# Kernel tuning notes

Measured on AMD Instinct MI355X. Metric: run time of the kernel, lower is better.

Reference implementation:

```python
import jax, jax.numpy as jnp
import numpy as np

N = 4096      # nodes (= attention seq_len)
D = 256       # dim_h
H = 4         # num_heads
HD = D // H   # head dim
E = 131072    # edges (avg degree 32)


def _ln(x, g, b, eps=1e-5):
    mu = jnp.mean(x, -1, keepdims=True)
    var = jnp.var(x, -1, keepdims=True)
    return (x - mu) * jax.lax.rsqrt(var + eps) * g + b


def setup_inputs() -> dict:
    key = jax.random.key(0)
    ks = jax.random.split(key, 10)
    s = 0.02
    nrm = lambda k, shape: jax.random.normal(k, shape, jnp.float32) * s
    return dict(
        x=jax.random.normal(ks[0], (N, D), jnp.float32),
        edge_index=jax.random.randint(ks[1], (2, E), 0, N, dtype=jnp.int32),
        W_gcn=nrm(ks[2], (D, D)), b_gcn=jnp.zeros((D,), jnp.float32),
        w_qkv=nrm(ks[3], (D, 3 * D)), b_qkv=jnp.zeros((3 * D,), jnp.float32),
        w_out=nrm(ks[4], (D, D)), b_out=jnp.zeros((D,), jnp.float32),
        g1l=jnp.ones((D,), jnp.float32), beta1l=jnp.zeros((D,), jnp.float32),
        g1a=jnp.ones((D,), jnp.float32), beta1a=jnp.zeros((D,), jnp.float32),
        W1=nrm(ks[5], (D, 2 * D)), bf1=jnp.zeros((2 * D,), jnp.float32),
        W2=nrm(ks[6], (2 * D, D)), bf2=jnp.zeros((D,), jnp.float32),
        g2=jnp.ones((D,), jnp.float32), beta2=jnp.zeros((D,), jnp.float32),
    )


def reference(x, edge_index, W_gcn, b_gcn, w_qkv, b_qkv, w_out, b_out,
              g1l, beta1l, g1a, beta1a, W1, bf1, W2, bf2, g2, beta2):
    n = x.shape[0]
    # --- GCNConv: sym-normalized aggregation with self loops ---
    loop = jnp.arange(n, dtype=edge_index.dtype)
    src = jnp.concatenate([edge_index[0], loop])
    dst = jnp.concatenate([edge_index[1], loop])
    deg = jax.ops.segment_sum(jnp.ones_like(src, x.dtype), dst, num_segments=n)
    dinv = jax.lax.rsqrt(deg)  # deg >= 1 thanks to self loops
    h = x @ W_gcn                                  # [N, D]
    msg = h[src] * (dinv[src] * dinv[dst])[:, None]  # gather + edge norm
    x_local = jax.ops.segment_sum(msg, dst, num_segments=n) + b_gcn
    x = _ln(x + x_local, g1l, beta1l)
    # --- Multi-head self-attention over all nodes (one sequence) ---
    qkv = x @ w_qkv + b_qkv
    q, k, v = jnp.split(qkv, 3, axis=-1)
    q = q.reshape(n, H, HD)
    k = k.reshape(n, H, HD)
    v = v.reshape(n, H, HD)
    scale = 1.0 / (HD ** 0.5)
    scores = jnp.einsum('nhd,mhd->hnm', q, k) * scale   # [H, N, N]
    attn = jax.nn.softmax(scores, axis=-1)
    x_attn = jnp.einsum('hnm,mhd->nhd', attn, v).reshape(n, D) @ w_out + b_out
    x = _ln(x + x_attn, g1a, beta1a)
    # --- FFN (D -> 2D -> D, ReLU) ---
    x_ffn = jax.nn.relu(x @ W1 + bf1) @ W2 + bf2
    return _ln(x + x_ffn, g2, beta2)
```

## Files before the change

kernel.cpp:

```cpp
#include <hip/hip_runtime.h>

typedef unsigned short u16;
typedef __bf16 bf16x8 __attribute__((ext_vector_type(8)));
typedef float f32x4 __attribute__((ext_vector_type(4)));

__device__ __forceinline__ u16 f2u(float f) {
    unsigned u = __builtin_bit_cast(unsigned, f);
    return (u16)((u + 0x7FFFu + ((u >> 16) & 1u)) >> 16);
}

__device__ __forceinline__ float u2f(u16 h) {
    return __builtin_bit_cast(float, (unsigned)h << 16);
}

__device__ __forceinline__ void glds16(const u16* g, u16* l) {
    __builtin_amdgcn_global_load_lds((const __attribute__((address_space(1))) unsigned int*)g,
                                     (__attribute__((address_space(3))) unsigned int*)l, 16, 0, 0);
}


__global__ __launch_bounds__(256) void prep_k(
    const float* __restrict__ w0, const float* __restrict__ w1, const float* __restrict__ w2,
    const float* __restrict__ w3, const float* __restrict__ w4, const float* __restrict__ x,
    u16* __restrict__ o0, u16* __restrict__ o1, u16* __restrict__ o2,
    u16* __restrict__ o3, u16* __restrict__ o4, u16* __restrict__ xo,
    int* __restrict__ cnt, int xblocks, int nn) {
    int b = blockIdx.x, t = threadIdx.x;
    if (b < 144) {
        const float* in; u16* out; int R, C, tb;
        if (b < 16)       { in = w0; out = o0; R = 256; C = 256; tb = b; }
        else if (b < 64)  { in = w1; out = o1; R = 256; C = 768; tb = b - 16; }
        else if (b < 80)  { in = w2; out = o2; R = 256; C = 256; tb = b - 64; }
        else if (b < 112) { in = w3; out = o3; R = 256; C = 512; tb = b - 80; }
        else              { in = w4; out = o4; R = 512; C = 256; tb = b - 112; }
        int tcols = C >> 6;
        int tr = tb / tcols, tc = tb - tr * tcols;
        __shared__ float T[64][65];
        int i0 = t >> 6, j = t & 63;
#pragma unroll
        for (int p = 0; p < 16; p++) {
            int r = p * 4 + i0;
            T[r][j] = in[(long)(tr * 64 + r) * C + tc * 64 + j];
        }
        __syncthreads();
#pragma unroll
        for (int p = 0; p < 16; p++) {
            int c = p * 4 + i0;
            out[(long)(tc * 64 + c) * R + tr * 64 + j] = f2u(T[j][c]);
        }
    } else if (b < 144 + xblocks) {
        long base = (long)(b - 144) * 4096;
#pragma unroll
        for (int p = 0; p < 4; p++) {
            long idx = base + p * 1024 + t * 4;
            float4 v = *(const float4*)&x[idx];
            unsigned lo = (unsigned)f2u(v.x) | ((unsigned)f2u(v.y) << 16);
            unsigned hi = (unsigned)f2u(v.z) | ((unsigned)f2u(v.w) << 16);
            *(uint2*)&xo[idx] = uint2{lo, hi};
        }
    } else {
        int i = (b - 144 - xblocks) * 256 + t;
        if (i < nn) cnt[i] = 0;
    }
}


__device__ __forceinline__ void block_ln_stats(float v, float& mu, float& rstd) {
    float s1 = v, s2 = v * v;
#pragma unroll
    for (int m = 1; m < 64; m <<= 1) { s1 += __shfl_xor(s1, m, 64); s2 += __shfl_xor(s2, m, 64); }
    __shared__ float r1[4], r2[4];
    int lane = threadIdx.x & 63, w = threadIdx.x >> 6;
    if (lane == 0) { r1[w] = s1; r2[w] = s2; }
    __syncthreads();
    s1 = r1[0] + r1[1] + r1[2] + r1[3];
    s2 = r2[0] + r2[1] + r2[2] + r2[3];
    mu = s1 * (1.0f / 256.0f);
    float var = s2 * (1.0f / 256.0f) - mu * mu;
    rstd = rsqrtf(var + 1e-5f);
}


__global__ __launch_bounds__(256) void gcn_agg_ln_k(
    const u16* __restrict__ h, const float* __restrict__ x,
    const int* __restrict__ srcs, const int* __restrict__ cnt,
    const float* __restrict__ bg,
    const float* __restrict__ g, const float* __restrict__ be,
    float* __restrict__ x1, u16* __restrict__ x1bf) {
    int n = blockIdx.x, d = threadIdx.x;
    int c = cnt[n]; c = c < 128 ? c : 128;
    int st = n << 7;
    float dn = rsqrtf((float)(c + 1));
    float agg = u2f(h[(long)n * 256 + d]) * dn;
    int e = 0;
    for (; e + 4 <= c; e += 4) {
        int s0 = srcs[st + e], s1 = srcs[st + e + 1], s2 = srcs[st + e + 2], s3 = srcs[st + e + 3];
        float a0 = u2f(h[(long)s0 * 256 + d]) * rsqrtf((float)(cnt[s0] + 1));
        float a1 = u2f(h[(long)s1 * 256 + d]) * rsqrtf((float)(cnt[s1] + 1));
        float a2 = u2f(h[(long)s2 * 256 + d]) * rsqrtf((float)(cnt[s2] + 1));
        float a3 = u2f(h[(long)s3 * 256 + d]) * rsqrtf((float)(cnt[s3] + 1));
        agg += (a0 + a1) + (a2 + a3);
    }
    for (; e < c; e++) {
        int s = srcs[st + e];
        agg += u2f(h[(long)s * 256 + d]) * rsqrtf((float)(cnt[s] + 1));
    }
    float v = x[(long)n * 256 + d] + dn * agg + bg[d];
    float mu, rs;
    block_ln_stats(v, mu, rs);
    float y = (v - mu) * rs * g[d] + be[d];
    x1[(long)n * 256 + d] = y;
    x1bf[(long)n * 256 + d] = f2u(y);
}


template <int EPI>
__device__ __forceinline__ void gemm_body(
    int bx, int by,
    const u16* __restrict__ A, const u16* __restrict__ Bt,
    const float* __restrict__ bias, void* __restrict__ outp,
    int M, int N, int K) {
    __shared__ __align__(16) u16 As[64 * 256];
    __shared__ __align__(16) u16 Bs[64 * 256];
    int tid = threadIdx.x;
    int lane = tid & 63, w = tid >> 6;
    int l15 = lane & 15, quad = lane >> 4, l7 = l15 & 7;
    int m0 = bx * 64, n0 = by * 64;
    int wm = (w >> 1) * 32, wn = (w & 1) * 32;
    f32x4 acc[2][2];
#pragma unroll
    for (int i = 0; i < 2; i++)
#pragma unroll
        for (int j = 0; j < 2; j++) acc[i][j] = f32x4{0.f, 0.f, 0.f, 0.f};

    int rA0 = (wm + l15) * 256, rA1 = (wm + 16 + l15) * 256;
    int rB0 = (wn + l15) * 256, rB1 = (wn + 16 + l15) * 256;

    for (int kb = 0; kb < K; kb += 256) {
        if (kb) __syncthreads();
#pragma unroll
        for (int i = 0; i < 8; i++) {
            int s = i * 256 + tid;
            int j = s >> 5, dch = s & 31;
            int c = dch ^ (j & 7);
            glds16(A + (long)(m0 + j) * K + kb + c * 8, &As[s * 8]);
            glds16(Bt + (long)(n0 + j) * K + kb + c * 8, &Bs[s * 8]);
        }
        __syncthreads();
#pragma unroll
        for (int step = 0; step < 8; step++) {
            int d8 = (((step << 2) + quad) ^ l7) << 3;
            bf16x8 af0 = *(const bf16x8*)&As[rA0 + d8];
            bf16x8 af1 = *(const bf16x8*)&As[rA1 + d8];
            bf16x8 bf0 = *(const bf16x8*)&Bs[rB0 + d8];
            bf16x8 bf1 = *(const bf16x8*)&Bs[rB1 + d8];
            acc[0][0] = __builtin_amdgcn_mfma_f32_16x16x32_bf16(af0, bf0, acc[0][0], 0, 0, 0);
            acc[0][1] = __builtin_amdgcn_mfma_f32_16x16x32_bf16(af0, bf1, acc[0][1], 0, 0, 0);
            acc[1][0] = __builtin_amdgcn_mfma_f32_16x16x32_bf16(af1, bf0, acc[1][0], 0, 0, 0);
            acc[1][1] = __builtin_amdgcn_mfma_f32_16x16x32_bf16(af1, bf1, acc[1][1], 0, 0, 0);
        }
    }

#pragma unroll
    for (int nf = 0; nf < 2; nf++) {
        int col = n0 + wn + nf * 16 + l15;
        float bv = bias ? bias[col] : 0.0f;
#pragma unroll
        for (int mf = 0; mf < 2; mf++) {
#pragma unroll
            for (int r = 0; r < 4; r++) {
                int row = m0 + wm + mf * 16 + quad * 4 + r;
                float v = acc[mf][nf][r] + bv;
                if (EPI == 1) {
                    u16* q = (u16*)outp;
                    u16* kk = q + (long)M * 256;
                    u16* vt = kk + (long)M * 256;
                    if (col < 256) {
                        q[(((col >> 6) * (long)M) + row) * 64 + (col & 63)] = f2u(v * 0.180336884f);
                    } else if (col < 512) {
                        int c = col - 256;
                        kk[(((c >> 6) * (long)M) + row) * 64 + (c & 63)] = f2u(v);
                    } else {
                        int c = col - 512;
                        vt[((c >> 6) * 64 + (c & 63)) * (long)M + row] = f2u(v);
                    }
                } else if (EPI == 2) {
                    ((u16*)outp)[(long)row * N + col] = f2u(v > 0.f ? v : 0.f);
                } else {
                    ((u16*)outp)[(long)row * N + col] = f2u(v);
                }
            }
        }
    }
}

template <int EPI>
__global__ __launch_bounds__(256) void gemm_k(
    const u16* __restrict__ A, const u16* __restrict__ Bt,
    const float* __restrict__ bias, void* __restrict__ outp,
    int M, int N, int K) {
    gemm_body<EPI>(blockIdx.x, blockIdx.y, A, Bt, bias, outp, M, N, K);
}


template <int WRITE_BF>
__global__ __launch_bounds__(256) void gemm_ln_k(
    const u16* __restrict__ A, const u16* __restrict__ Bt, const float* __restrict__ bias,
    const float* __restrict__ res, const float* __restrict__ g, const float* __restrict__ be,
    float* __restrict__ outf, u16* __restrict__ outbf, int M, int K) {
    __shared__ __align__(16) u16 As[16 * 64];
    __shared__ __align__(16) u16 Bs[256 * 64];
    __shared__ float red[2][4][16];
    int tid = threadIdx.x;
    int lane = tid & 63, w = tid >> 6;
    int l15 = lane & 15, quad = lane >> 4, l7 = l15 & 7;
    int m0 = blockIdx.x * 16;
    f32x4 acc[4];
#pragma unroll
    for (int i = 0; i < 4; i++) acc[i] = f32x4{0.f, 0.f, 0.f, 0.f};

    int jA = tid >> 3, dA = tid & 7, cA = dA ^ (jA & 7);
    const u16* agp = A + (long)(m0 + jA) * K + cA * 8;

    for (int kb = 0; kb < K; kb += 64) {
        if (kb) __syncthreads();
        if (tid < 128) glds16(agp + kb, &As[tid * 8]);
#pragma unroll
        for (int i = 0; i < 8; i++) {
            int s = i * 256 + tid;
            int jb = s >> 3, db = s & 7, cb = db ^ (jb & 7);
            glds16(Bt + (long)jb * K + kb + cb * 8, &Bs[s * 8]);
        }
        __syncthreads();
#pragma unroll
        for (int step = 0; step < 2; step++) {
            int d8 = (((step << 2) + quad) ^ l7) << 3;
            bf16x8 af = *(const bf16x8*)&As[l15 * 64 + d8];
#pragma unroll
            for (int nf = 0; nf < 4; nf++) {
                int rb = w * 64 + nf * 16 + l15;
                bf16x8 bfr = *(const bf16x8*)&Bs[rb * 64 + d8];
                acc[nf] = __builtin_amdgcn_mfma_f32_16x16x32_bf16(af, bfr, acc[nf], 0, 0, 0);
            }
        }
    }

    float vv[4][4];
    float p1[4] = {0.f, 0.f, 0.f, 0.f}, p2[4] = {0.f, 0.f, 0.f, 0.f};
#pragma unroll
    for (int nf = 0; nf < 4; nf++) {
        int col = w * 64 + nf * 16 + l15;
        float bv = bias[col];
#pragma unroll
        for (int r = 0; r < 4; r++) {
            int row = m0 + quad * 4 + r;
            float v = acc[nf][r] + bv + res[(long)row * 256 + col];
            vv[nf][r] = v;
            p1[r] += v; p2[r] += v * v;
        }
    }
#pragma unroll
    for (int m = 1; m < 16; m <<= 1) {
#pragma unroll
        for (int r = 0; r < 4; r++) {
            p1[r] += __shfl_xor(p1[r], m, 64);
            p2[r] += __shfl_xor(p2[r], m, 64);
        }
    }
    if (l15 == 0) {
#pragma unroll
        for (int r = 0; r < 4; r++) { red[0][w][quad * 4 + r] = p1[r]; red[1][w][quad * 4 + r] = p2[r]; }
    }
    __syncthreads();
    float mu[4], rs[4];
#pragma unroll
    for (int r = 0; r < 4; r++) {
        int rr = quad * 4 + r;
        float s1 = red[0][0][rr] + red[0][1][rr] + red[0][2][rr] + red[0][3][rr];
        float s2 = red[1][0][rr] + red[1][1][rr] + red[1][2][rr] + red[1][3][rr];
        mu[r] = s1 * (1.0f / 256.0f);
        float var = s2 * (1.0f / 256.0f) - mu[r] * mu[r];
        rs[r] = rsqrtf(var + 1e-5f);
    }
#pragma unroll
    for (int nf = 0; nf < 4; nf++) {
        int col = w * 64 + nf * 16 + l15;
        float gg = g[col], bb = be[col];
#pragma unroll
        for (int r = 0; r < 4; r++) {
            int row = m0 + quad * 4 + r;
            float y = (vv[nf][r] - mu[r]) * rs[r] * gg + bb;
            outf[(long)row * 256 + col] = y;
            if (WRITE_BF) outbf[(long)row * 256 + col] = f2u(y);
        }
    }
}


__global__ __launch_bounds__(256) void front_k(
    const int* __restrict__ ei, int E, int* __restrict__ cnt, int* __restrict__ srcs,
    const u16* __restrict__ A, const u16* __restrict__ Bt, void* __restrict__ outp,
    int M, int N, int K, int SB) {
    int b = blockIdx.x;
    if (b < SB) {
        int e = b * 256 + threadIdx.x;
        if (e < E) {
            int s = ei[e], d = ei[E + e];
            int p = atomicAdd(&cnt[d], 1);
            if (p < 128) srcs[(d << 7) + p] = s;
        }
    } else {
        int id = b - SB;
        gemm_body<3>(id & 63, id >> 6, A, Bt, nullptr, outp, M, N, K);
    }
}


__global__ __launch_bounds__(256) void attn_k(const u16* __restrict__ qg, const u16* __restrict__ kg,
                                              const u16* __restrict__ vtg, float* __restrict__ po,
                                              float* __restrict__ pl, int N, int S) {
    int tid = threadIdx.x;
    int w = tid >> 6, lane = tid & 63, l15 = lane & 15, quad = lane >> 4;
    int lid = blockIdx.x + 64 * blockIdx.y + 256 * blockIdx.z;
    int hs = lid & 7;
    int hh = hs & 3, sp = hs >> 2, qb = lid >> 3;
    int q0 = qb * 64 + w * 16;
    int kbeg = sp * (N / S);
    int nit = (N / S) / 64;
    const u16* qh = qg + (long)hh * N * 64;
    const u16* kh = kg + (long)hh * N * 64;
    const u16* vh = vtg + (long)hh * 64 * N;

    __shared__ __align__(16) u16 KV[2][2][4096];
    __shared__ __align__(16) u16 P[4][1024];
    u16* Pw = &P[w][0];

    int s0 = tid, j0 = s0 >> 3, c0s = ((s0 & 7) ^ (j0 & 7)) * 8;
    int s1 = tid + 256, j1 = s1 >> 3, c1s = ((s1 & 7) ^ (j1 & 7)) * 8;
    const u16* kp0 = kh + (long)(kbeg + j0) * 64 + c0s;
    const u16* kp1 = kh + (long)(kbeg + j1) * 64 + c1s;
    const u16* vp0 = vh + (long)j0 * N + kbeg + c0s;
    const u16* vp1 = vh + (long)j1 * N + kbeg + c1s;
    u16* lk0[2] = {&KV[0][0][s0 * 8], &KV[1][0][s0 * 8]};
    u16* lk1[2] = {&KV[0][0][s1 * 8], &KV[1][0][s1 * 8]};
    u16* lv0[2] = {&KV[0][1][s0 * 8], &KV[1][1][s0 * 8]};
    u16* lv1[2] = {&KV[0][1][s1 * 8], &KV[1][1][s1 * 8]};

    int lo3 = l15 & 7;
    int c0 = (quad ^ lo3) * 8;
    int c1 = c0 ^ 32;
    int ps = lo3 << 1;
    int pw0 = l15 * 64 + (((quad << 1) ^ ps) << 2);
    int pw1 = l15 * 64 + (((8 + (quad << 1)) ^ ps) << 2);
    int pca[4];
#pragma unroll
    for (int nt = 0; nt < 4; nt++) pca[nt] = l15 * 64 + (((nt * 4 + quad) ^ ps) << 2);

    bf16x8 aq0 = *(const bf16x8*)(qh + (long)(q0 + l15) * 64 + quad * 8);
    bf16x8 aq1 = *(const bf16x8*)(qh + (long)(q0 + l15) * 64 + 32 + quad * 8);
    bf16x8 ones;
#pragma unroll
    for (int i = 0; i < 8; i++) ones[i] = (__bf16)1.0f;

    f32x4 o[4];
#pragma unroll
    for (int dn = 0; dn < 4; dn++) o[dn] = f32x4{0.f, 0.f, 0.f, 0.f};
    f32x4 accl = f32x4{0.f, 0.f, 0.f, 0.f};

    glds16(kp0, lk0[0]); glds16(kp1, lk1[0]);
    glds16(vp0, lv0[0]); glds16(vp1, lv1[0]);
    kp0 += 4096; kp1 += 4096; vp0 += 64; vp1 += 64;

    for (int it = 0; it < nit; it++) {
        __syncthreads();
        if (it + 1 < nit) {
            int nb = (it + 1) & 1;
            glds16(kp0, lk0[nb]); glds16(kp1, lk1[nb]);
            glds16(vp0, lv0[nb]); glds16(vp1, lv1[nb]);
            kp0 += 4096; kp1 += 4096; vp0 += 64; vp1 += 64;
        }
        const u16* Kc = &KV[it & 1][0][0];
        const u16* Vc = &KV[it & 1][1][0];
#pragma unroll
        for (int nt = 0; nt < 4; nt++) {
            const u16* Kr = Kc + (nt * 16 + l15) * 64;
            bf16x8 kf0 = *(const bf16x8*)(Kr + c0);
            bf16x8 kf1 = *(const bf16x8*)(Kr + c1);
            f32x4 s = f32x4{0.f, 0.f, 0.f, 0.f};
            s = __builtin_amdgcn_mfma_f32_16x16x32_bf16(kf0, aq0, s, 0, 0, 0);
            s = __builtin_amdgcn_mfma_f32_16x16x32_bf16(kf1, aq1, s, 0, 0, 0);
            unsigned u0 = (unsigned)((int)(s[0] * 8388608.0f) + 1064992209);
            unsigned u1 = (unsigned)((int)(s[1] * 8388608.0f) + 1064992209);
            unsigned u2 = (unsigned)((int)(s[2] * 8388608.0f) + 1064992209);
            unsigned u3 = (unsigned)((int)(s[3] * 8388608.0f) + 1064992209);
            unsigned pk01 = __builtin_amdgcn_perm(u1, u0, 0x07060302u);
            unsigned pk23 = __builtin_amdgcn_perm(u3, u2, 0x07060302u);
            *(uint2*)&Pw[pca[nt]] = uint2{pk01, pk23};
        }
        bf16x8 pa0 = *(const bf16x8*)&Pw[pw0];
        bf16x8 pa1 = *(const bf16x8*)&Pw[pw1];
        accl = __builtin_amdgcn_mfma_f32_16x16x32_bf16(pa0, ones, accl, 0, 0, 0);
        accl = __builtin_amdgcn_mfma_f32_16x16x32_bf16(pa1, ones, accl, 0, 0, 0);
#pragma unroll
        for (int dn = 0; dn < 4; dn++) {
            const u16* Vr = Vc + (dn * 16 + l15) * 64;
            bf16x8 v0 = *(const bf16x8*)(Vr + c0);
            bf16x8 v1 = *(const bf16x8*)(Vr + c1);
            o[dn] = __builtin_amdgcn_mfma_f32_16x16x32_bf16(pa0, v0, o[dn], 0, 0, 0);
            o[dn] = __builtin_amdgcn_mfma_f32_16x16x32_bf16(pa1, v1, o[dn], 0, 0, 0);
        }
    }

    long pbase = ((long)(sp * 4 + hh)) * N;
#pragma unroll
    for (int dn = 0; dn < 4; dn++)
#pragma unroll
        for (int r = 0; r < 4; r++) {
            int row = q0 + quad * 4 + r;
            po[(pbase + row) * 64 + dn * 16 + l15] = o[dn][r];
        }
    if (l15 == 0) {
#pragma unroll
        for (int r = 0; r < 4; r++) pl[pbase + q0 + quad * 4 + r] = accl[r];
    }
}

__global__ __launch_bounds__(256) void attn_comb_k(const float* __restrict__ po, const float* __restrict__ pl,
                                                   u16* __restrict__ xo, int N, int S) {
    int n = blockIdx.x, c = threadIdx.x;
    int hh = c >> 6, d = c & 63;
    float osum = 0.f, lsum = 0.f;
    for (int s = 0; s < S; s++) {
        osum += po[(((long)(s * 4 + hh)) * N + n) * 64 + d];
        lsum += pl[((long)(s * 4 + hh)) * N + n];
    }
    xo[(long)n * 256 + c] = f2u(osum / lsum);
}


extern "C" void kernel_launch(void* const* d_in, const int* in_sizes, int n_in,
                              void* d_out, int out_size, void* d_ws, size_t ws_size,
                              hipStream_t stream) {
    const float* x    = (const float*)d_in[0];
    const int*   ei   = (const int*)d_in[1];
    const float* Wg   = (const float*)d_in[2];
    const float* bg   = (const float*)d_in[3];
    const float* Wqkv = (const float*)d_in[4];
    const float* bqkv = (const float*)d_in[5];
    const float* Wo   = (const float*)d_in[6];
    const float* bo   = (const float*)d_in[7];
    const float* g1l  = (const float*)d_in[8];
    const float* b1l  = (const float*)d_in[9];
    const float* g1a  = (const float*)d_in[10];
    const float* b1a  = (const float*)d_in[11];
    const float* W1   = (const float*)d_in[12];
    const float* bf1  = (const float*)d_in[13];
    const float* W2   = (const float*)d_in[14];
    const float* bf2  = (const float*)d_in[15];
    const float* g2   = (const float*)d_in[16];
    const float* b2   = (const float*)d_in[17];
    float* out = (float*)d_out;

    int N = in_sizes[0] / 256;
    int E = in_sizes[1] / 2;
    const int S = 2;

    char* p = (char*)d_ws;
    auto alloc = [&](size_t bytes) { void* r = (void*)p; p += (bytes + 255) & ~(size_t)255; return r; };
    u16*   wg_t   = (u16*)alloc((size_t)256 * 256 * 2);
    u16*   wqkv_t = (u16*)alloc((size_t)256 * 768 * 2);
    u16*   wo_t   = (u16*)alloc((size_t)256 * 256 * 2);
    u16*   w1_t   = (u16*)alloc((size_t)512 * 256 * 2);
    u16*   w2_t   = (u16*)alloc((size_t)256 * 512 * 2);
    u16*   xbf    = (u16*)alloc((size_t)N * 256 * 2);
    u16*   h      = (u16*)alloc((size_t)N * 256 * 2);
    int*   cnt    = (int*)alloc((size_t)N * 4);
    int*   srcs   = (int*)alloc((size_t)N * 128 * 4);
    float* x1     = (float*)alloc((size_t)N * 256 * 4);
    u16*   x1bf   = (u16*)alloc((size_t)N * 256 * 2);
    u16*   qkv    = (u16*)alloc((size_t)3 * N * 256 * 2);
    u16*   xattn  = (u16*)alloc((size_t)N * 256 * 2);
    float* x2     = (float*)alloc((size_t)N * 256 * 4);
    u16*   x2bf   = (u16*)alloc((size_t)N * 256 * 2);
    u16*   ffn1   = (u16*)alloc((size_t)N * 512 * 2);
    float* po     = (float*)alloc((size_t)S * 4 * N * 64 * 4);
    float* pl     = (float*)alloc((size_t)S * 4 * N * 4);

    dim3 b256(256);

    int xblocks = (N * 256) / 4096;
    int cblocks = (N + 255) / 256;
    prep_k<<<144 + xblocks + cblocks, b256, 0, stream>>>(Wg, Wqkv, Wo, W1, W2, x,
                                                         wg_t, wqkv_t, wo_t, w1_t, w2_t, xbf,
                                                         cnt, xblocks, N);

    int SB = (E + 255) / 256;
    front_k<<<SB + (N / 64) * 4, b256, 0, stream>>>(ei, E, cnt, srcs, xbf, wg_t, h, N, 256, 256, SB);

    gcn_agg_ln_k<<<N, b256, 0, stream>>>(h, x, srcs, cnt, bg, g1l, b1l, x1, x1bf);

    gemm_k<1><<<dim3(N / 64, 12), b256, 0, stream>>>(x1bf, wqkv_t, bqkv, qkv, N, 768, 256);
    attn_k<<<dim3(N / 64, 4, S), b256, 0, stream>>>(qkv, qkv + (size_t)N * 256, qkv + (size_t)2 * N * 256,
                                                    po, pl, N, S);
    attn_comb_k<<<N, b256, 0, stream>>>(po, pl, xattn, N, S);

    gemm_ln_k<1><<<N / 16, b256, 0, stream>>>(xattn, wo_t, bo, x1, g1a, b1a, x2, x2bf, N, 256);

    gemm_k<2><<<dim3(N / 64, 8), b256, 0, stream>>>(x2bf, w1_t, bf1, ffn1, N, 512, 256);

    gemm_ln_k<0><<<N / 16, b256, 0, stream>>>(ffn1, w2_t, bf2, x2, g2, b2, out, nullptr, N, 512);
}
```

Baseline: 195.0 us.

## Use 32x32x16 MFMA in attention with register-resident probabilities via permlane32 swap

Rewrites the attention kernel to use 32x32x16 bf16 MFMA tiles, with 32 query rows per wave and 128 per block. The probability tile no longer goes through LDS: it is reshaped in registers with v_permlane32_swap. The row-sum is accumulated with scalar adds instead of an MFMA against a ones vector. The key split S goes from 2 to 4 to keep enough blocks in flight, at the cost of more partial outputs for the combine kernel to read and reduce.

```diff
diff --git a/kernel.cpp b/kernel.cpp
--- a/kernel.cpp
+++ b/kernel.cpp
@@ -3,6 +3,8 @@
 typedef unsigned short u16;
 typedef __bf16 bf16x8 __attribute__((ext_vector_type(8)));
 typedef float f32x4 __attribute__((ext_vector_type(4)));
+typedef float f32x16 __attribute__((ext_vector_type(16)));
+typedef unsigned u32x4v __attribute__((ext_vector_type(4)));
 
 __device__ __forceinline__ u16 f2u(float f) {
     unsigned u = __builtin_bit_cast(unsigned, f);
@@ -320,11 +322,10 @@
                                               const u16* __restrict__ vtg, float* __restrict__ po,
                                               float* __restrict__ pl, int N, int S) {
     int tid = threadIdx.x;
-    int w = tid >> 6, lane = tid & 63, l15 = lane & 15, quad = lane >> 4;
-    int lid = blockIdx.x + 64 * blockIdx.y + 256 * blockIdx.z;
-    int hs = lid & 7;
-    int hh = hs & 3, sp = hs >> 2, qb = lid >> 3;
-    int q0 = qb * 64 + w * 16;
+    int w = tid >> 6, lane = tid & 63;
+    int l31 = lane & 31, h = lane >> 5, xr = l31 & 7;
+    int hh = blockIdx.y, sp = blockIdx.z;
+    int q0w = blockIdx.x * 128 + w * 32;
     int kbeg = sp * (N / S);
     int nit = (N / S) / 64;
     const u16* qh = qg + (long)hh * N * 64;
@@ -332,8 +333,6 @@
     const u16* vh = vtg + (long)hh * 64 * N;
 
     __shared__ __align__(16) u16 KV[2][2][4096];
-    __shared__ __align__(16) u16 P[4][1024];
-    u16* Pw = &P[w][0];
 
     int s0 = tid, j0 = s0 >> 3, c0s = ((s0 & 7) ^ (j0 & 7)) * 8;
     int s1 = tid + 256, j1 = s1 >> 3, c1s = ((s1 & 7) ^ (j1 & 7)) * 8;
@@ -346,26 +345,13 @@
     u16* lv0[2] = {&KV[0][1][s0 * 8], &KV[1][1][s0 * 8]};
     u16* lv1[2] = {&KV[0][1][s1 * 8], &KV[1][1][s1 * 8]};
 
-    int lo3 = l15 & 7;
-    int c0 = (quad ^ lo3) * 8;
-    int c1 = c0 ^ 32;
-    int ps = lo3 << 1;
-    int pw0 = l15 * 64 + (((quad << 1) ^ ps) << 2);
-    int pw1 = l15 * 64 + (((8 + (quad << 1)) ^ ps) << 2);
-    int pca[4];
-#pragma unroll
-    for (int nt = 0; nt < 4; nt++) pca[nt] = l15 * 64 + (((nt * 4 + quad) ^ ps) << 2);
-
-    bf16x8 aq0 = *(const bf16x8*)(qh + (long)(q0 + l15) * 64 + quad * 8);
-    bf16x8 aq1 = *(const bf16x8*)(qh + (long)(q0 + l15) * 64 + 32 + quad * 8);
-    bf16x8 ones;
-#pragma unroll
-    for (int i = 0; i < 8; i++) ones[i] = (__bf16)1.0f;
-
-    f32x4 o[4];
-#pragma unroll
-    for (int dn = 0; dn < 4; dn++) o[dn] = f32x4{0.f, 0.f, 0.f, 0.f};
-    f32x4 accl = f32x4{0.f, 0.f, 0.f, 0.f};
+    bf16x8 qf[4];
+#pragma unroll
+    for (int stp = 0; stp < 4; stp++)
+        qf[stp] = *(const bf16x8*)(qh + (long)(q0w + l31) * 64 + stp * 16 + h * 8);
+
+    f32x16 o0{}, o1{};
+    float ll = 0.f;
 
     glds16(kp0, lk0[0]); glds16(kp1, lk1[0]);
     glds16(vp0, lv0[0]); glds16(vp1, lv1[0]);
@@ -381,48 +367,65 @@
         }
         const u16* Kc = &KV[it & 1][0][0];
         const u16* Vc = &KV[it & 1][1][0];
-#pragma unroll
-        for (int nt = 0; nt < 4; nt++) {
-            const u16* Kr = Kc + (nt * 16 + l15) * 64;
-            bf16x8 kf0 = *(const bf16x8*)(Kr + c0);
-            bf16x8 kf1 = *(const bf16x8*)(Kr + c1);
-            f32x4 s = f32x4{0.f, 0.f, 0.f, 0.f};
-            s = __builtin_amdgcn_mfma_f32_16x16x32_bf16(kf0, aq0, s, 0, 0, 0);
-            s = __builtin_amdgcn_mfma_f32_16x16x32_bf16(kf1, aq1, s, 0, 0, 0);
-            unsigned u0 = (unsigned)((int)(s[0] * 8388608.0f) + 1064992209);
-            unsigned u1 = (unsigned)((int)(s[1] * 8388608.0f) + 1064992209);
-            unsigned u2 = (unsigned)((int)(s[2] * 8388608.0f) + 1064992209);
-            unsigned u3 = (unsigned)((int)(s[3] * 8388608.0f) + 1064992209);
-            unsigned pk01 = __builtin_amdgcn_perm(u1, u0, 0x07060302u);
-            unsigned pk23 = __builtin_amdgcn_perm(u3, u2, 0x07060302u);
-            *(uint2*)&Pw[pca[nt]] = uint2{pk01, pk23};
-        }
-        bf16x8 pa0 = *(const bf16x8*)&Pw[pw0];
-        bf16x8 pa1 = *(const bf16x8*)&Pw[pw1];
-        accl = __builtin_amdgcn_mfma_f32_16x16x32_bf16(pa0, ones, accl, 0, 0, 0);
-        accl = __builtin_amdgcn_mfma_f32_16x16x32_bf16(pa1, ones, accl, 0, 0, 0);
-#pragma unroll
-        for (int dn = 0; dn < 4; dn++) {
-            const u16* Vr = Vc + (dn * 16 + l15) * 64;
-            bf16x8 v0 = *(const bf16x8*)(Vr + c0);
-            bf16x8 v1 = *(const bf16x8*)(Vr + c1);
-            o[dn] = __builtin_amdgcn_mfma_f32_16x16x32_bf16(pa0, v0, o[dn], 0, 0, 0);
-            o[dn] = __builtin_amdgcn_mfma_f32_16x16x32_bf16(pa1, v1, o[dn], 0, 0, 0);
-        }
-    }
-
+
+        f32x16 sA{}, sB{};
+#pragma unroll
+        for (int stp = 0; stp < 4; stp++) {
+            int cc = (((stp << 1) + h) ^ xr) * 8;
+            bf16x8 kfa = *(const bf16x8*)&Kc[l31 * 64 + cc];
+            bf16x8 kfb = *(const bf16x8*)&Kc[(32 + l31) * 64 + cc];
+            sA = __builtin_amdgcn_mfma_f32_32x32x16_bf16(kfa, qf[stp], sA, 0, 0, 0);
+            sB = __builtin_amdgcn_mfma_f32_32x32x16_bf16(kfb, qf[stp], sB, 0, 0, 0);
+        }
+
+#pragma unroll
+        for (int kt = 0; kt < 2; kt++) {
+            f32x16 s = kt ? sB : sA;
+            unsigned wr[8];
+#pragma unroll
+            for (int i = 0; i < 8; i++) {
+                unsigned ua = (unsigned)((int)(s[2 * i] * 8388608.0f) + 1064992209);
+                unsigned ub = (unsigned)((int)(s[2 * i + 1] * 8388608.0f) + 1064992209);
+                ll += __builtin_bit_cast(float, ua & 0xffff0000u);
+                ll += __builtin_bit_cast(float, ub & 0xffff0000u);
+                wr[i] = __builtin_amdgcn_perm(ub, ua, 0x07060302u);
+            }
+            asm("v_permlane32_swap_b32 %0, %1" : "+v"(wr[2]), "+v"(wr[0]));
+            asm("v_permlane32_swap_b32 %0, %1" : "+v"(wr[3]), "+v"(wr[1]));
+            asm("v_permlane32_swap_b32 %0, %1" : "+v"(wr[6]), "+v"(wr[4]));
+            asm("v_permlane32_swap_b32 %0, %1" : "+v"(wr[7]), "+v"(wr[5]));
+            u32x4v t0 = {wr[0], wr[1], wr[2], wr[3]};
+            u32x4v t1 = {wr[4], wr[5], wr[6], wr[7]};
+            bf16x8 f0 = __builtin_bit_cast(bf16x8, t0);
+            bf16x8 f1 = __builtin_bit_cast(bf16x8, t1);
+
+#pragma unroll
+            for (int dt = 0; dt < 2; dt++) {
+                int rowb = (dt * 32 + l31) * 64;
+                bf16x8 v0 = *(const bf16x8*)&Vc[rowb + (((kt << 2) + h) ^ xr) * 8];
+                bf16x8 v1 = *(const bf16x8*)&Vc[rowb + (((kt << 2) + 2 + h) ^ xr) * 8];
+                if (dt == 0) {
+                    o0 = __builtin_amdgcn_mfma_f32_32x32x16_bf16(f0, v0, o0, 0, 0, 0);
+                    o0 = __builtin_amdgcn_mfma_f32_32x32x16_bf16(f1, v1, o0, 0, 0, 0);
+                } else {
+                    o1 = __builtin_amdgcn_mfma_f32_32x32x16_bf16(f0, v0, o1, 0, 0, 0);
+                    o1 = __builtin_amdgcn_mfma_f32_32x32x16_bf16(f1, v1, o1, 0, 0, 0);
+                }
+            }
+        }
+    }
+
+    ll += __shfl_xor(ll, 32, 64);
     long pbase = ((long)(sp * 4 + hh)) * N;
 #pragma unroll
-    for (int dn = 0; dn < 4; dn++)
-#pragma unroll
-        for (int r = 0; r < 4; r++) {
-            int row = q0 + quad * 4 + r;
-            po[(pbase + row) * 64 + dn * 16 + l15] = o[dn][r];
-        }
-    if (l15 == 0) {
-#pragma unroll
-        for (int r = 0; r < 4; r++) pl[pbase + q0 + quad * 4 + r] = accl[r];
-    }
+    for (int dt = 0; dt < 2; dt++)
+#pragma unroll
+        for (int r = 0; r < 16; r++) {
+            int qrow = q0w + (r & 3) + ((r >> 2) << 3) + (h << 2);
+            float val = dt ? o1[r] : o0[r];
+            po[(pbase + qrow) * 64 + dt * 32 + l31] = val;
+        }
+    if (lane < 32) pl[pbase + q0w + lane] = ll;
 }
 
 __global__ __launch_bounds__(256) void attn_comb_k(const float* __restrict__ po, const float* __restrict__ pl,
@@ -463,7 +466,7 @@
 
     int N = in_sizes[0] / 256;
     int E = in_sizes[1] / 2;
-    const int S = 2;
+    const int S = 4;
 
     char* p = (char*)d_ws;
     auto alloc = [&](size_t bytes) { void* r = (void*)p; p += (bytes + 255) & ~(size_t)255; return r; };
@@ -500,8 +503,8 @@
     gcn_agg_ln_k<<<N, b256, 0, stream>>>(h, x, srcs, cnt, bg, g1l, b1l, x1, x1bf);
 
     gemm_k<1><<<dim3(N / 64, 12), b256, 0, stream>>>(x1bf, wqkv_t, bqkv, qkv, N, 768, 256);
-    attn_k<<<dim3(N / 64, 4, S), b256, 0, stream>>>(qkv, qkv + (size_t)N * 256, qkv + (size_t)2 * N * 256,
-                                                    po, pl, N, S);
+    attn_k<<<dim3(N / 128, 4, S), b256, 0, stream>>>(qkv, qkv + (size_t)N * 256, qkv + (size_t)2 * N * 256,
+                                                     po, pl, N, S);
     attn_comb_k<<<N, b256, 0, stream>>>(po, pl, xattn, N, S);
 
     gemm_ln_k<1><<<N / 16, b256, 0, stream>>>(xattn, wo_t, bo, x1, g1a, b1a, x2, x2bf, N, 256);
```

Result: faster. 187.2 us (-4.0%).
